# Optimization experiments

Measured on AMD Instinct MI355X. Metric: run time of the kernel, lower is better.

Reference implementation:

```python
import jax, jax.numpy as jnp
import numpy as np

N0, N1 = 30000, 20000
N = N0 + N1
E = 400000
H0, H1, H2 = 4, 4, 1
DH = 64            # num_hidden
NC = 16            # num_classes
IN = 128           # per-type input feature dim
SLOPE = 0.2        # leaky relu negative slope


def setup_inputs() -> dict:
    key = jax.random.key(0)
    ks = iter(jax.random.split(key, 48))
    rn = lambda shape, s=0.05: jax.random.normal(next(ks), shape, jnp.float32) * s
    ri = lambda shape: jax.random.randint(next(ks), shape, 0, N, jnp.int32)
    inp = {
        'features0': rn((N0, IN), 1.0),
        'features1': rn((N1, IN), 1.0),
        'fc_w0': rn((IN, DH)), 'fc_b0': jnp.zeros((DH,), jnp.float32),
        'fc_w1': rn((IN, DH)), 'fc_b1': jnp.zeros((DH,), jnp.float32),
        'mix_w': jnp.zeros((2, 3, 2), jnp.float32),  # (n_types, num_layers+1, n_graphs)
        # GATConv params stacked over the 2 relation graphs
        'W0': rn((2, DH, H0 * DH)), 'al0': rn((2, H0, DH), 0.1), 'ar0': rn((2, H0, DH), 0.1), 'b0': jnp.zeros((2, H0 * DH), jnp.float32),
        'W1': rn((2, H0 * DH, H1 * DH)), 'al1': rn((2, H1, DH), 0.1), 'ar1': rn((2, H1, DH), 0.1), 'b1': jnp.zeros((2, H1 * DH), jnp.float32),
        'W2': rn((2, H1 * DH, H2 * NC)), 'al2': rn((2, H2, NC), 0.1), 'ar2': rn((2, H2, NC), 0.1), 'b2': jnp.zeros((2, H2 * NC), jnp.float32),
        'res2': rn((2, H1 * DH, H2 * NC)),  # res_fc for last layer (in != out*heads)
        'src0': ri((E,)), 'dst0': ri((E,)),
        'src1': ri((E,)), 'dst1': ri((E,)),
    }
    return inp


def gat_conv(h, src, dst, W, al, ar, b, H, D, res_mode, res_w, act):
    # h: (N, in)  ->  (N, H, D)
    feat = (h @ W).reshape(N, H, D)
    el = jnp.sum(feat * al, axis=-1)   # (N, H)
    er = jnp.sum(feat * ar, axis=-1)   # (N, H)
    e = jax.nn.leaky_relu(el[src] + er[dst], SLOPE)  # (E, H)
    # edge softmax over incoming edges of each dst node
    m = jax.ops.segment_max(e, dst, num_segments=N)
    ex = jnp.exp(e - m[dst])
    den = jax.ops.segment_sum(ex, dst, num_segments=N)
    alpha = ex / den[dst]                              # (E, H)
    out = jax.ops.segment_sum(feat[src] * alpha[..., None], dst, num_segments=N)
    if res_mode == 'id':
        out = out + h.reshape(N, H, D)
    elif res_mode == 'fc':
        out = out + (h @ res_w).reshape(N, H, D)
    out = out + b.reshape(1, H, D)
    return jax.nn.elu(out) if act else out


def _forward(features0, features1, fc_w0, fc_b0, fc_w1, fc_b1, mix_w,
             W0, al0, ar0, b0, W1, al1, ar1, b1, W2, al2, ar2, b2, res2,
             src0, dst0, src1, dst1):
    nt = jnp.concatenate([jnp.zeros(N0, jnp.int32), jnp.ones(N1, jnp.int32)])
    w = jax.nn.softmax(mix_w, axis=2)  # (types, layers+1, graphs)
    h = jnp.concatenate([features0 @ fc_w0 + fc_b0, features1 @ fc_w1 + fc_b1], axis=0)
    srcs, dsts = (src0, src1), (dst0, dst1)
    layers = [
        (W0, al0, ar0, b0, H0, DH, None, True),
        (W1, al1, ar1, b1, H1, DH, 'id', True),
    ]
    for l, (W, al, ar, b, H, D, rm, act) in enumerate(layers):
        acc = 0.
        for i in range(2):
            o = gat_conv(h, srcs[i], dsts[i], W[i], al[i], ar[i], b[i], H, D, rm, None, act)
            acc = acc + o.reshape(N, H * D) * w[nt, l, i][:, None]
        h = acc
    logits = 0.
    for i in range(2):
        o = gat_conv(h, srcs[i], dsts[i], W2[i], al2[i], ar2[i], b2[i], H2, NC, 'fc', res2[i], False)
        logits = logits + o.mean(axis=1) * w[nt, 2, i][:, None]
    return logits


def reference(features0, features1, fc_w0, fc_b0, fc_w1, fc_b1, mix_w,
              W0, al0, ar0, b0, W1, al1, ar1, b1, W2, al2, ar2, b2, res2,
              src0, dst0, src1, dst1):
    return _forward(features0, features1, fc_w0, fc_b0, fc_w1, fc_b1, mix_w,
                    W0, al0, ar0, b0, W1, al1, ar1, b1, W2, al2, ar2, b2, res2,
                    src0, dst0, src1, dst1)
```

## Files before the change

kernel.cpp:

```cpp
#include <hip/hip_runtime.h>
#include <hip/hip_bf16.h>

#define NN   50000
#define NN0  30000
#define EE   400000
#define NB_SCAN ((NN + 1023) / 1024)
#define NRT   3125
#define NGRP  ((NRT + 3) / 4)

typedef unsigned short u16;
typedef unsigned int   u32;

typedef __attribute__((ext_vector_type(8))) __bf16 bf16x8;
typedef __attribute__((ext_vector_type(4))) float  f32x4;

__device__ __forceinline__ float bf2f(u16 u){ return __uint_as_float(((u32)u)<<16); }
__device__ __forceinline__ float lo16(u32 u){ return __uint_as_float(u<<16); }
__device__ __forceinline__ float hi16(u32 u){ return __uint_as_float(u & 0xffff0000u); }
__device__ __forceinline__ u16 f2bf(float f){
  u32 x = __float_as_uint(f);
  x += 0x7fffu + ((x>>16)&1u);
  return (u16)(x>>16);
}
__device__ __forceinline__ float elu_f(float x){ return x>0.f ? x : __expf(x)-1.f; }
__device__ __forceinline__ float lrelu(float x){ return x>0.f ? x : 0.2f*x; }
__device__ __forceinline__ bf16x8 ld_frag(const u16* p){
  uint4 v = *(const uint4*)p;
  return __builtin_bit_cast(bf16x8, v);
}

__global__ __launch_bounds__(256) void k_prep(
    const float* __restrict__ mix_w, float* __restrict__ wsoft,
    const float* __restrict__ W0, u16* __restrict__ W0p,
    const float* __restrict__ W1, u16* __restrict__ W1p,
    const float* __restrict__ W2, const float* __restrict__ res2, u16* __restrict__ W2p)
{
  int t = blockIdx.x*256 + threadIdx.x;
  if (t < 6){
    float a0 = mix_w[t*2+0], a1 = mix_w[t*2+1];
    float mx = fmaxf(a0,a1);
    float e0 = __expf(a0-mx), e1 = __expf(a1-mx);
    wsoft[t*2+0] = e0/(e0+e1); wsoft[t*2+1] = e1/(e0+e1);
  }
  if (t < 4096){
    int gg = t>>11, fi = t&2047;
    int lane = fi&63, kb = (fi>>6)&1, ct = fi>>7;
    int q = lane>>4, c = lane&15;
    const float* src = W0 + (size_t)gg*64*256;
    u16* o = W0p + (size_t)gg*16384 + (size_t)fi*8;
    #pragma unroll
    for (int j=0;j<8;j++) o[j] = f2bf(src[(size_t)(kb*32+q*8+j)*256 + ct*16 + c]);
  } else if (t < 20480){
    int u = t - 4096;
    int gg = u>>13, fi = u&8191;
    int lane = fi&63, kb = (fi>>6)&7, ct = fi>>9;
    int q = lane>>4, c = lane&15;
    const float* src = W1 + (size_t)gg*65536;
    u16* o = W1p + (size_t)gg*65536 + (size_t)fi*8;
    #pragma unroll
    for (int j=0;j<8;j++) o[j] = f2bf(src[(size_t)(kb*32+q*8+j)*256 + ct*16 + c]);
  } else if (t < 22528){
    int fi = t - 20480;
    int lane = fi&63, kb = (fi>>6)&7, ct = fi>>9;
    int q = lane>>4, c = lane&15;
    int cl = ct*16 + c;
    int i = cl>>5, which = (cl>>4)&1;
    const float* src = which ? res2 : W2;
    u16* o = W2p + (size_t)fi*8;
    #pragma unroll
    for (int j=0;j<8;j++) o[j] = f2bf(src[(size_t)i*4096 + (size_t)(kb*32+q*8+j)*16 + (cl&15)]);
  }
}

__global__ void k_count2(const int* __restrict__ d0, const int* __restrict__ d1,
                         int* __restrict__ cnt2){
  int t = blockIdx.x*256 + threadIdx.x;
  int g = blockIdx.y;
  if (t < EE) atomicAdd(&cnt2[g*NN + (g ? d1[t] : d0[t])], 1);
}

__global__ __launch_bounds__(1024) void k_scan1(const int* __restrict__ cnt2,
                                                int* __restrict__ row2, int* __restrict__ bsum){
  __shared__ int wsum[16];
  int g = blockIdx.y;
  int lane = threadIdx.x & 63, wid = threadIdx.x >> 6;
  int i = blockIdx.x*1024 + threadIdx.x;
  int v = (i < NN) ? cnt2[g*NN + i] : 0;
  int x = v;
  #pragma unroll
  for (int off = 1; off < 64; off <<= 1){
    int y = __shfl_up(x, off, 64);
    if (lane >= off) x += y;
  }
  if (lane == 63) wsum[wid] = x;
  __syncthreads();
  if (wid == 0 && lane < 16){
    int s = wsum[lane];
    #pragma unroll
    for (int off = 1; off < 16; off <<= 1){
      int y = __shfl_up(s, off, 16);
      if (lane >= off) s += y;
    }
    wsum[lane] = s;
  }
  __syncthreads();
  int incl = x + (wid ? wsum[wid-1] : 0);
  if (i < NN) row2[(size_t)g*(NN+1) + i] = incl - v;
  if (threadIdx.x == 1023) bsum[g*NB_SCAN + blockIdx.x] = incl;
}

__global__ __launch_bounds__(128) void k_scan2(const int* __restrict__ bsum, int* __restrict__ boff){
  int g = threadIdx.x >> 6, lane = threadIdx.x & 63;
  int v = (lane < NB_SCAN) ? bsum[g*NB_SCAN + lane] : 0;
  int x = v;
  #pragma unroll
  for (int off = 1; off < 64; off <<= 1){
    int y = __shfl_up(x, off, 64);
    if (lane >= off) x += y;
  }
  if (lane < NB_SCAN) boff[g*NB_SCAN + lane] = x - v;
}

__global__ __launch_bounds__(1024) void k_scan3(int* __restrict__ row2, const int* __restrict__ boff){
  int g = blockIdx.y;
  int i = blockIdx.x*1024 + threadIdx.x;
  if (i < NN) row2[(size_t)g*(NN+1) + i] += boff[g*NB_SCAN + blockIdx.x];
  if (blockIdx.x == 0 && threadIdx.x == 0) row2[(size_t)g*(NN+1) + NN] = EE;
}

__global__ void k_scatter2(const int* __restrict__ s0, const int* __restrict__ d0,
                           const int* __restrict__ s1, const int* __restrict__ d1,
                           const int* __restrict__ row2, int* __restrict__ fill2,
                           int* __restrict__ col2){
  int t = blockIdx.x*256 + threadIdx.x;
  int g = blockIdx.y;
  if (t >= EE) return;
  int d = g ? d1[t] : d0[t];
  int s = g ? s1[t] : s0[t];
  int pos = atomicAdd(&fill2[g*NN + d], 1);
  col2[(size_t)g*EE + row2[(size_t)g*(NN+1) + d] + pos] = s;
}

__global__ __launch_bounds__(256) void k_in_proj(
    const float* __restrict__ f0, const float* __restrict__ f1,
    const float* __restrict__ w0, const float* __restrict__ b0,
    const float* __restrict__ w1, const float* __restrict__ b1,
    u16* __restrict__ h)
{
  __shared__ float fs[4][128];
  int wv = threadIdx.x>>6, ln = threadIdx.x&63;
  int n = blockIdx.x*4 + wv;
  const float *fr, *W, *B;
  if (n < NN0){ fr = f0 + (size_t)n*128; W=w0; B=b0; }
  else        { fr = f1 + (size_t)(n-NN0)*128; W=w1; B=b1; }
  float2 u = ((const float2*)fr)[ln];
  fs[wv][2*ln]   = u.x;
  fs[wv][2*ln+1] = u.y;
  __syncthreads();
  float acc = B[ln];
  #pragma unroll 8
  for (int k=0;k<128;k++) acc = fmaf(fs[wv][k], W[k*64+ln], acc);
  h[(size_t)n*64 + ln] = f2bf(acc);
}

template<int K>
__global__ __launch_bounds__(256) void k_gemm4(
    const u16* __restrict__ A,
    const u16* __restrict__ Bp, size_t bpStride,
    const float* __restrict__ al, const float* __restrict__ ar, int alStride,
    u16* __restrict__ feat, size_t featStride,
    float* __restrict__ el, float* __restrict__ er, size_t elStride)
{
  constexpr int KB = K/32;
  int wv = threadIdx.x>>6, ln = threadIdx.x&63;
  int bid = blockIdx.x;
  int g = bid / NGRP, grp = bid % NGRP;
  int split = wv, q = ln>>4, c = ln&15;
  const u16* Bpg = Bp + (size_t)g*bpStride;
  const float* alg = al + (size_t)g*alStride;
  const float* arg = ar + (size_t)g*alStride;
  u16* featg = feat + (size_t)g*featStride;
  float* elg = el + (size_t)g*elStride;
  float* erg = er + (size_t)g*elStride;

  f32x4 acc[4][4] = {};
  int  tbase = grp*4;
  bool valid[4];
  const u16* Ap[4];
  #pragma unroll
  for (int rt=0; rt<4; rt++){
    int ti = tbase + rt;
    valid[rt] = (ti < NRT);
    if (!valid[rt]) ti = NRT-1;
    Ap[rt] = A + (size_t)(ti*16 + c)*K + q*8;
  }
  const u16* Bbase = Bpg + ((size_t)(split*4)*KB*64 + ln)*8;

  #pragma unroll 2
  for (int kb=0; kb<KB; kb++){
    bf16x8 b[4], a[4];
    #pragma unroll
    for (int ct=0; ct<4; ct++) b[ct] = ld_frag(Bbase + (size_t)(ct*KB + kb)*64*8);
    #pragma unroll
    for (int rt=0; rt<4; rt++) a[rt] = ld_frag(Ap[rt] + kb*32);
    #pragma unroll
    for (int rt=0; rt<4; rt++)
      #pragma unroll
      for (int ct=0; ct<4; ct++)
        acc[rt][ct] = __builtin_amdgcn_mfma_f32_16x16x32_bf16(a[rt], b[ct], acc[rt][ct], 0,0,0);
  }

  float alv[4], arv[4];
  #pragma unroll
  for (int ct=0;ct<4;ct++){
    int cg = (split*4+ct)*16 + c;
    alv[ct] = alg[cg]; arv[ct] = arg[cg];
  }
  #pragma unroll
  for (int rt=0; rt<4; rt++){
    if (!valid[rt]) continue;
    int row0 = (tbase+rt)*16;
    #pragma unroll
    for (int j=0;j<4;j++){
      float ep=0.f, rp=0.f;
      #pragma unroll
      for (int ct=0;ct<4;ct++){ ep += acc[rt][ct][j]*alv[ct]; rp += acc[rt][ct][j]*arv[ct]; }
      #pragma unroll
      for (int off=8; off; off>>=1){ ep += __shfl_xor(ep,off,16); rp += __shfl_xor(rp,off,16); }
      int row = row0 + q*4 + j;
      if (c==0){ elg[row*4+split]=ep; erg[row*4+split]=rp; }
      #pragma unroll
      for (int ct=0;ct<4;ct++)
        featg[(size_t)row*256 + (split*4+ct)*16 + c] = f2bf(acc[rt][ct][j]);
    }
  }
}

template<int RES>
__global__ __launch_bounds__(256) void k_aggNF(
    const int* __restrict__ row2, const int* __restrict__ col2,
    const u16* __restrict__ feat, size_t featStride,
    const float* __restrict__ el, const float* __restrict__ er, size_t elStride,
    const u16* __restrict__ hres, const float* __restrict__ bias,
    const float* __restrict__ wsoft, int l,
    u16* __restrict__ hout)
{
  int wv = threadIdx.x>>6, ln = threadIdx.x&63;
  int n = blockIdx.x*4 + wv;
  int h = ln>>4;
  int type = (n<NN0)?0:1;
  float rx=0.f, ry=0.f, rz=0.f, rw_=0.f;
  if (RES){
    uint2 r = ((const uint2*)hres)[(size_t)n*64 + ln];
    rx=lo16(r.x); ry=hi16(r.x); rz=lo16(r.y); rw_=hi16(r.y);
  }
  float o0=0.f,o1=0.f,o2=0.f,o3=0.f;
  #pragma unroll
  for (int g=0; g<2; g++){
    const int* rw = row2 + (size_t)g*(NN+1);
    const int* cl = col2 + (size_t)g*EE;
    const uint2* fp = (const uint2*)(feat + (size_t)g*featStride);
    const float* elg = el + (size_t)g*elStride;
    float er_h = (er + (size_t)g*elStride)[n*4+h];
    int beg = rw[n], end = rw[n+1];
    float den = 0.f;
    float a0=0.f,a1=0.f,a2=0.f,a3=0.f;
    int k = beg;
    for (; k+4<=end; k+=4){
      int s0=cl[k], s1=cl[k+1], s2=cl[k+2], s3=cl[k+3];
      float x0 = __expf(lrelu(elg[s0*4+h] + er_h));
      float x1 = __expf(lrelu(elg[s1*4+h] + er_h));
      float x2 = __expf(lrelu(elg[s2*4+h] + er_h));
      float x3 = __expf(lrelu(elg[s3*4+h] + er_h));
      uint2 f0 = fp[(size_t)s0*64 + ln];
      uint2 f1 = fp[(size_t)s1*64 + ln];
      uint2 f2 = fp[(size_t)s2*64 + ln];
      uint2 f3 = fp[(size_t)s3*64 + ln];
      den += (x0+x1) + (x2+x3);
      a0 += x0*lo16(f0.x) + x1*lo16(f1.x) + x2*lo16(f2.x) + x3*lo16(f3.x);
      a1 += x0*hi16(f0.x) + x1*hi16(f1.x) + x2*hi16(f2.x) + x3*hi16(f3.x);
      a2 += x0*lo16(f0.y) + x1*lo16(f1.y) + x2*lo16(f2.y) + x3*lo16(f3.y);
      a3 += x0*hi16(f0.y) + x1*hi16(f1.y) + x2*hi16(f2.y) + x3*hi16(f3.y);
    }
    for (; k<end; k++){
      int s = cl[k];
      float x = __expf(lrelu(elg[s*4+h] + er_h));
      uint2 f = fp[(size_t)s*64 + ln];
      den += x;
      a0 += x*lo16(f.x); a1 += x*hi16(f.x); a2 += x*lo16(f.y); a3 += x*hi16(f.y);
    }
    float inv = (end>beg) ? 1.0f/den : 0.f;
    float4 bv = ((const float4*)(bias + g*256))[ln];
    a0 = a0*inv + bv.x; a1 = a1*inv + bv.y; a2 = a2*inv + bv.z; a3 = a3*inv + bv.w;
    if (RES){ a0 += rx; a1 += ry; a2 += rz; a3 += rw_; }
    float w = wsoft[type*6 + l*2 + g];
    o0 += w*elu_f(a0); o1 += w*elu_f(a1); o2 += w*elu_f(a2); o3 += w*elu_f(a3);
  }
  uint2 o;
  o.x = (u32)f2bf(o0) | ((u32)f2bf(o1)<<16);
  o.y = (u32)f2bf(o2) | ((u32)f2bf(o3)<<16);
  ((uint2*)hout)[(size_t)n*64 + ln] = o;
}

template<int RES>
__global__ __launch_bounds__(256) void k_aggN(
    const int* __restrict__ row, const int* __restrict__ col,
    const u16* __restrict__ feat, const float* __restrict__ el, const float* __restrict__ er,
    const u16* __restrict__ hres, const float* __restrict__ bias,
    const float* __restrict__ wsoft, int l, int i, int first,
    u16* __restrict__ hout)
{
  int wv = threadIdx.x>>6, ln = threadIdx.x&63;
  int n = blockIdx.x*4 + wv;
  int h = ln>>4;
  int beg = row[n], end = row[n+1];
  float er_h = er[n*4+h];
  const uint2* fp = (const uint2*)feat;
  float den = 0.f;
  float a0=0.f,a1=0.f,a2=0.f,a3=0.f;
  int k = beg;
  for (; k+4<=end; k+=4){
    int s0=col[k], s1=col[k+1], s2=col[k+2], s3=col[k+3];
    float x0 = __expf(lrelu(el[s0*4+h] + er_h));
    float x1 = __expf(lrelu(el[s1*4+h] + er_h));
    float x2 = __expf(lrelu(el[s2*4+h] + er_h));
    float x3 = __expf(lrelu(el[s3*4+h] + er_h));
    uint2 f0 = fp[(size_t)s0*64 + ln];
    uint2 f1 = fp[(size_t)s1*64 + ln];
    uint2 f2 = fp[(size_t)s2*64 + ln];
    uint2 f3 = fp[(size_t)s3*64 + ln];
    den += (x0+x1) + (x2+x3);
    a0 += x0*lo16(f0.x) + x1*lo16(f1.x) + x2*lo16(f2.x) + x3*lo16(f3.x);
    a1 += x0*hi16(f0.x) + x1*hi16(f1.x) + x2*hi16(f2.x) + x3*hi16(f3.x);
    a2 += x0*lo16(f0.y) + x1*lo16(f1.y) + x2*lo16(f2.y) + x3*lo16(f3.y);
    a3 += x0*hi16(f0.y) + x1*hi16(f1.y) + x2*hi16(f2.y) + x3*hi16(f3.y);
  }
  for (; k<end; k++){
    int s = col[k];
    float x = __expf(lrelu(el[s*4+h] + er_h));
    uint2 f = fp[(size_t)s*64 + ln];
    den += x;
    a0 += x*lo16(f.x); a1 += x*hi16(f.x); a2 += x*lo16(f.y); a3 += x*hi16(f.y);
  }
  float inv = (end>beg) ? 1.0f/den : 0.f;
  a0 *= inv; a1 *= inv; a2 *= inv; a3 *= inv;
  float4 bv = ((const float4*)bias)[ln];
  a0 += bv.x; a1 += bv.y; a2 += bv.z; a3 += bv.w;
  if (RES){
    uint2 r = ((const uint2*)hres)[(size_t)n*64 + ln];
    a0 += lo16(r.x); a1 += hi16(r.x); a2 += lo16(r.y); a3 += hi16(r.y);
  }
  a0 = elu_f(a0); a1 = elu_f(a1); a2 = elu_f(a2); a3 = elu_f(a3);
  float w = wsoft[((n<NN0)?0:1)*6 + l*2 + i];
  a0 *= w; a1 *= w; a2 *= w; a3 *= w;
  if (!first){
    uint2 p = ((const uint2*)hout)[(size_t)n*64 + ln];
    a0 += lo16(p.x); a1 += hi16(p.x); a2 += lo16(p.y); a3 += hi16(p.y);
  }
  uint2 o;
  o.x = (u32)f2bf(a0) | ((u32)f2bf(a1)<<16);
  o.y = (u32)f2bf(a2) | ((u32)f2bf(a3)<<16);
  ((uint2*)hout)[(size_t)n*64 + ln] = o;
}

__global__ __launch_bounds__(256) void k_gemm2(
    const u16* __restrict__ A, const u16* __restrict__ Bp,
    const float* __restrict__ al2, const float* __restrict__ ar2,
    float* __restrict__ feat16, float* __restrict__ resb,
    float* __restrict__ el2, float* __restrict__ er2)
{
  int wv = threadIdx.x>>6, ln = threadIdx.x&63;
  int wt = blockIdx.x*4 + wv;
  if (wt >= NN/16) return;
  int row0 = wt*16;
  int q = ln>>4, c = ln&15;
  f32x4 acc[4] = {};
  const u16* Ap = A + (size_t)(row0 + c)*256 + q*8;
  #pragma unroll
  for (int kb=0; kb<8; kb++){
    bf16x8 a = ld_frag(Ap + kb*32);
    #pragma unroll
    for (int t=0;t<4;t++){
      bf16x8 b = ld_frag(Bp + ((size_t)(t*8 + kb)*64 + ln)*8);
      acc[t] = __builtin_amdgcn_mfma_f32_16x16x32_bf16(a, b, acc[t], 0,0,0);
    }
  }
  #pragma unroll
  for (int i=0;i<2;i++){
    float alv = al2[i*16+c], arv = ar2[i*16+c];
    #pragma unroll
    for (int j=0;j<4;j++){
      float ep = acc[2*i][j]*alv, rp = acc[2*i][j]*arv;
      #pragma unroll
      for (int off=8; off; off>>=1){ ep += __shfl_xor(ep,off,16); rp += __shfl_xor(rp,off,16); }
      if (c==0){
        int row = row0 + q*4 + j;
        el2[(size_t)i*NN + row] = ep; er2[(size_t)i*NN + row] = rp;
      }
    }
    #pragma unroll
    for (int j=0;j<4;j++){
      int row = row0 + q*4 + j;
      feat16[(size_t)i*NN*16 + (size_t)row*16 + c] = acc[2*i][j];
      resb  [(size_t)i*NN*16 + (size_t)row*16 + c] = acc[2*i+1][j];
    }
  }
}

__global__ __launch_bounds__(256) void k_agg2D(
    const int* __restrict__ row2, const int* __restrict__ col2,
    const float* __restrict__ feat16, const float* __restrict__ el2,
    const float* __restrict__ er2, const float* __restrict__ resb,
    const float* __restrict__ b2, const float* __restrict__ wsoft,
    float* __restrict__ out)
{
  int t = threadIdx.x;
  int nl = t>>4, j = t&15;
  int n = blockIdx.x*16 + nl;
  int type = (n<NN0)?0:1;
  float o = 0.f;
  #pragma unroll
  for (int i=0;i<2;i++){
    const int* rw = row2 + (size_t)i*(NN+1);
    const int* cl = col2 + (size_t)i*EE;
    const float* f  = feat16 + (size_t)i*NN*16;
    const float* eli= el2 + (size_t)i*NN;
    float ern = er2[(size_t)i*NN + n];
    int beg = rw[n], end = rw[n+1];
    float den = 0.f, acc = 0.f;
    int k = beg;
    for (; k+4<=end; k+=4){
      int s0=cl[k], s1=cl[k+1], s2=cl[k+2], s3=cl[k+3];
      float x0 = __expf(lrelu(eli[s0] + ern));
      float x1 = __expf(lrelu(eli[s1] + ern));
      float x2 = __expf(lrelu(eli[s2] + ern));
      float x3 = __expf(lrelu(eli[s3] + ern));
      float v0 = f[(size_t)s0*16 + j];
      float v1 = f[(size_t)s1*16 + j];
      float v2 = f[(size_t)s2*16 + j];
      float v3 = f[(size_t)s3*16 + j];
      den += (x0+x1) + (x2+x3);
      acc += x0*v0 + x1*v1 + x2*v2 + x3*v3;
    }
    for (; k<end; k++){
      int s = cl[k];
      float x = __expf(lrelu(eli[s] + ern));
      den += x;
      acc = fmaf(x, f[(size_t)s*16 + j], acc);
    }
    float inv = (end>beg) ? 1.0f/den : 0.f;
    float oi = acc*inv + b2[i*16+j] + resb[(size_t)i*NN*16 + (size_t)n*16 + j];
    o += oi * wsoft[type*6 + 4 + i];
  }
  out[(size_t)n*16 + j] = o;
}

extern "C" void kernel_launch(void* const* d_in, const int* in_sizes, int n_in,
                              void* d_out, int out_size, void* d_ws, size_t ws_size,
                              hipStream_t stream)
{
  const float* features0 = (const float*)d_in[0];
  const float* features1 = (const float*)d_in[1];
  const float* fc_w0 = (const float*)d_in[2];
  const float* fc_b0 = (const float*)d_in[3];
  const float* fc_w1 = (const float*)d_in[4];
  const float* fc_b1 = (const float*)d_in[5];
  const float* mix_w = (const float*)d_in[6];
  const float* W0  = (const float*)d_in[7];
  const float* al0 = (const float*)d_in[8];
  const float* ar0 = (const float*)d_in[9];
  const float* b0  = (const float*)d_in[10];
  const float* W1  = (const float*)d_in[11];
  const float* al1 = (const float*)d_in[12];
  const float* ar1 = (const float*)d_in[13];
  const float* b1  = (const float*)d_in[14];
  const float* W2  = (const float*)d_in[15];
  const float* al2 = (const float*)d_in[16];
  const float* ar2 = (const float*)d_in[17];
  const float* b2  = (const float*)d_in[18];
  const float* res2= (const float*)d_in[19];
  const int* src[2] = {(const int*)d_in[20], (const int*)d_in[22]};
  const int* dst[2] = {(const int*)d_in[21], (const int*)d_in[23]};
  (void)in_sizes; (void)n_in; (void)out_size;

  char* ws = (char*)d_ws;
  size_t off = 0;
  auto alloc = [&](size_t bytes)->char*{
    char* p = ws + off; off += (bytes + 255) & ~(size_t)255; return p;
  };
  float* wsoft = (float*)alloc(64*4);
  u16*   W0p   = (u16*)  alloc((size_t)2*64*256*2);
  u16*   W1p   = (u16*)  alloc((size_t)2*256*256*2);
  u16*   W2p   = (u16*)  alloc((size_t)256*64*2);
  int*   row2  = (int*)  alloc((size_t)2*(NN+1)*4);
  int*   col2  = (int*)  alloc((size_t)2*EE*4);
  int*   zeros = (int*)  alloc((size_t)4*NN*4);
  int*   cnt2  = zeros;
  int*   fill2 = zeros + 2*NN;
  int*   bsum  = (int*)alloc((size_t)2*NB_SCAN*4);
  int*   boff  = (int*)alloc((size_t)2*NB_SCAN*4);
  u16*   h0    = (u16*)alloc((size_t)NN*64*2);
  u16*   h1    = (u16*)alloc((size_t)NN*256*2);
  u16*   h2    = (u16*)alloc((size_t)NN*256*2);
  float* elA   = (float*)alloc((size_t)2*NN*4*4);
  float* erA   = (float*)alloc((size_t)2*NN*4*4);
  size_t featBytes1 = (size_t)NN*256*2;
  size_t off_D = off;
  bool fused = (ws_size >= off_D + 2*featBytes1 + (16<<20));
  u16* featD = (u16*)alloc(fused ? 2*featBytes1 : featBytes1);
  float* feat16 = (float*)(ws + off_D);
  float* resb   = feat16 + (size_t)2*NN*16;
  float* el2    = resb   + (size_t)2*NN*16;
  float* er2    = el2    + (size_t)2*NN;

  k_prep<<<(22528+255)/256,256,0,stream>>>(mix_w, wsoft, W0, W0p, W1, W1p, W2, res2, W2p);

  hipMemsetAsync(zeros, 0, (size_t)4*NN*4, stream);
  {
    dim3 gE((EE+255)/256, 2), gS(NB_SCAN, 2);
    k_count2 <<<gE,256,0,stream>>>(dst[0], dst[1], cnt2);
    k_scan1  <<<gS,1024,0,stream>>>(cnt2, row2, bsum);
    k_scan2  <<<1,128,0,stream>>>(bsum, boff);
    k_scan3  <<<gS,1024,0,stream>>>(row2, boff);
    k_scatter2<<<gE,256,0,stream>>>(src[0], dst[0], src[1], dst[1], row2, fill2, col2);
  }

  k_in_proj<<<NN/4,256,0,stream>>>(features0, features1, fc_w0, fc_b0, fc_w1, fc_b1, h0);

  if (fused){
    k_gemm4<64><<<2*NGRP,256,0,stream>>>(h0, W0p, (size_t)64*256, al0, ar0, 256,
                                         featD, featBytes1/2, elA, erA, (size_t)NN*4);
    k_aggNF<0><<<NN/4,256,0,stream>>>(row2, col2, featD, featBytes1/2, elA, erA, (size_t)NN*4,
                                      (const u16*)nullptr, b0, wsoft, 0, h1);
    k_gemm4<256><<<2*NGRP,256,0,stream>>>(h1, W1p, (size_t)256*256, al1, ar1, 256,
                                          featD, featBytes1/2, elA, erA, (size_t)NN*4);
    k_aggNF<1><<<NN/4,256,0,stream>>>(row2, col2, featD, featBytes1/2, elA, erA, (size_t)NN*4,
                                      h1, b1, wsoft, 1, h2);
  } else {
    for (int i=0;i<2;i++){
      k_gemm4<64><<<NGRP,256,0,stream>>>(h0, W0p+(size_t)i*64*256, 0, al0+i*256, ar0+i*256, 0,
                                         featD, 0, elA, erA, 0);
      k_aggN<0><<<NN/4,256,0,stream>>>(row2+(size_t)i*(NN+1), col2+(size_t)i*EE, featD, elA, erA,
                                       (const u16*)nullptr, b0+i*256, wsoft, 0, i, (i==0)?1:0, h1);
    }
    for (int i=0;i<2;i++){
      k_gemm4<256><<<NGRP,256,0,stream>>>(h1, W1p+(size_t)i*256*256, 0, al1+i*256, ar1+i*256, 0,
                                          featD, 0, elA, erA, 0);
      k_aggN<1><<<NN/4,256,0,stream>>>(row2+(size_t)i*(NN+1), col2+(size_t)i*EE, featD, elA, erA,
                                       h1, b1+i*256, wsoft, 1, i, (i==0)?1:0, h2);
    }
  }

  k_gemm2<<<(NN/16+3)/4,256,0,stream>>>(h2, W2p, al2, ar2, feat16, resb, el2, er2);
  k_agg2D<<<NN/16,256,0,stream>>>(row2, col2, feat16, el2, er2, resb, b2, wsoft, (float*)d_out);
}
```

Before: 496.8 us.

## Aggregate layer-0 in 64-dim input space before projecting with W0

Layer 0 now aggregates the 64-wide h0 features per head (edge softmax applied) and only then multiplies by W0, using linearity of the projection. The attention logits el/er come from h0 through precomputed folded vectors W0·al / W0·ar, so the 256-wide per-graph feature tensor is no longer gathered during aggregation. The input projection moves to MFMA bf16, which converts the features to bf16 on the fly. The change adds an intermediate aggB buffer, three kernels replacing two, and removes the non-fused fallback path, so the fused workspace size is now assumed.

Measured after the change: 465.9 us. 1.07x faster.

```diff
diff --git a/kernel.cpp b/kernel.cpp
--- a/kernel.cpp
+++ b/kernel.cpp
@@ -7,6 +7,7 @@
 #define NB_SCAN ((NN + 1023) / 1024)
 #define NRT   3125
 #define NGRP  ((NRT + 3) / 4)
+#define NT0   1875
 
 typedef unsigned short u16;
 typedef unsigned int   u32;
@@ -28,12 +29,24 @@
   uint4 v = *(const uint4*)p;
   return __builtin_bit_cast(bf16x8, v);
 }
+__device__ __forceinline__ bf16x8 cvt8(const float* p){
+  float4 u = ((const float4*)p)[0];
+  float4 v = ((const float4*)p)[1];
+  u32 w0 = (u32)f2bf(u.x) | ((u32)f2bf(u.y)<<16);
+  u32 w1 = (u32)f2bf(u.z) | ((u32)f2bf(u.w)<<16);
+  u32 w2 = (u32)f2bf(v.x) | ((u32)f2bf(v.y)<<16);
+  u32 w3 = (u32)f2bf(v.z) | ((u32)f2bf(v.w)<<16);
+  uint4 r{w0,w1,w2,w3};
+  return __builtin_bit_cast(bf16x8, r);
+}
 
 __global__ __launch_bounds__(256) void k_prep(
     const float* __restrict__ mix_w, float* __restrict__ wsoft,
     const float* __restrict__ W0, u16* __restrict__ W0p,
     const float* __restrict__ W1, u16* __restrict__ W1p,
-    const float* __restrict__ W2, const float* __restrict__ res2, u16* __restrict__ W2p)
+    const float* __restrict__ W2, const float* __restrict__ res2, u16* __restrict__ W2p,
+    const float* __restrict__ fcw0, const float* __restrict__ fcw1, u16* __restrict__ Fp,
+    const float* __restrict__ al0, const float* __restrict__ ar0, u16* __restrict__ Vp)
 {
   int t = blockIdx.x*256 + threadIdx.x;
   if (t < 6){
@@ -46,7 +59,7 @@
     int gg = t>>11, fi = t&2047;
     int lane = fi&63, kb = (fi>>6)&1, ct = fi>>7;
     int q = lane>>4, c = lane&15;
-    const float* src = W0 + (size_t)gg*64*256;
+    const float* src = W0 + (size_t)gg*16384;
     u16* o = W0p + (size_t)gg*16384 + (size_t)fi*8;
     #pragma unroll
     for (int j=0;j<8;j++) o[j] = f2bf(src[(size_t)(kb*32+q*8+j)*256 + ct*16 + c]);
@@ -69,6 +82,28 @@
     u16* o = W2p + (size_t)fi*8;
     #pragma unroll
     for (int j=0;j<8;j++) o[j] = f2bf(src[(size_t)i*4096 + (size_t)(kb*32+q*8+j)*16 + (cl&15)]);
+  } else if (t < 24576){
+    int u = t - 22528;
+    int tt = u>>10, fi = u&1023;
+    int lane = fi&63, kb = (fi>>6)&3, ct = fi>>8;
+    int q = lane>>4, c = lane&15;
+    const float* src = tt ? fcw1 : fcw0;
+    u16* o = Fp + (size_t)tt*8192 + (size_t)fi*8;
+    #pragma unroll
+    for (int j=0;j<8;j++) o[j] = f2bf(src[(size_t)(kb*32+q*8+j)*64 + ct*16 + c]);
+  } else if (t < 25600){
+    int u = t - 24576;
+    int fi = u>>3, j = u&7;
+    int lane = fi&63, kb = fi>>6;
+    int q = lane>>4, c = lane&15;
+    int k = kb*32 + q*8 + j;
+    int which = c>>3, g=(c>>2)&1, h=c&3;
+    const float* sel = (which ? ar0 : al0) + (size_t)(g*4+h)*64;
+    const float* Wrow = W0 + (size_t)g*16384 + (size_t)k*256 + h*64;
+    float s=0.f;
+    #pragma unroll 8
+    for (int d=0;d<64;d++) s = fmaf(Wrow[d], sel[d], s);
+    Vp[(size_t)fi*8 + j] = f2bf(s);
   }
 }
 
@@ -141,26 +176,158 @@
   col2[(size_t)g*EE + row2[(size_t)g*(NN+1) + d] + pos] = s;
 }
 
-__global__ __launch_bounds__(256) void k_in_proj(
+__global__ __launch_bounds__(256) void k_inproj_m(
     const float* __restrict__ f0, const float* __restrict__ f1,
-    const float* __restrict__ w0, const float* __restrict__ b0,
-    const float* __restrict__ w1, const float* __restrict__ b1,
-    u16* __restrict__ h)
-{
-  __shared__ float fs[4][128];
+    const u16* __restrict__ Fp, const float* __restrict__ fb0, const float* __restrict__ fb1,
+    u16* __restrict__ h0)
+{
+  int wv = threadIdx.x>>6, ln = threadIdx.x&63;
+  int ti = blockIdx.x*4 + wv;
+  if (ti >= NRT) return;
+  int q = ln>>4, c = ln&15;
+  int type = (ti < NT0) ? 0 : 1;
+  const float* F = type ? f1 : f0;
+  int rbase = type ? (ti*16 - NN0) : ti*16;
+  const u16* Bg = Fp + (size_t)type*8192;
+  const float* bb = type ? fb1 : fb0;
+  f32x4 acc[4] = {};
+  const float* Ap = F + (size_t)(rbase + c)*128;
+  #pragma unroll
+  for (int kb=0; kb<4; kb++){
+    bf16x8 a = cvt8(Ap + kb*32 + q*8);
+    #pragma unroll
+    for (int ct=0; ct<4; ct++){
+      bf16x8 b = ld_frag(Bg + ((size_t)(ct*4+kb)*64 + ln)*8);
+      acc[ct] = __builtin_amdgcn_mfma_f32_16x16x32_bf16(a, b, acc[ct], 0,0,0);
+    }
+  }
+  #pragma unroll
+  for (int ct=0; ct<4; ct++){
+    float bv = bb[ct*16+c];
+    #pragma unroll
+    for (int j=0;j<4;j++){
+      int row = ti*16 + q*4 + j;
+      h0[(size_t)row*64 + ct*16 + c] = f2bf(acc[ct][j] + bv);
+    }
+  }
+}
+
+__global__ __launch_bounds__(256) void k_eler0(
+    const u16* __restrict__ h0, const u16* __restrict__ Vp,
+    float* __restrict__ elA, float* __restrict__ erA)
+{
+  int wv = threadIdx.x>>6, ln = threadIdx.x&63;
+  int ti = blockIdx.x*4 + wv;
+  if (ti >= NRT) return;
+  int q = ln>>4, c = ln&15;
+  f32x4 acc = {};
+  const u16* Ap = h0 + (size_t)(ti*16 + c)*64 + q*8;
+  #pragma unroll
+  for (int kb=0; kb<2; kb++){
+    bf16x8 a = ld_frag(Ap + kb*32);
+    bf16x8 b = ld_frag(Vp + ((size_t)(kb*64 + ln))*8);
+    acc = __builtin_amdgcn_mfma_f32_16x16x32_bf16(a, b, acc, 0,0,0);
+  }
+  int which = c>>3, g = (c>>2)&1, h = c&3;
+  float* dst = (which ? erA : elA) + (size_t)g*NN*4;
+  #pragma unroll
+  for (int j=0;j<4;j++){
+    int row = ti*16 + q*4 + j;
+    dst[row*4 + h] = acc[j];
+  }
+}
+
+__global__ __launch_bounds__(256) void k_agg0(
+    const int* __restrict__ row2, const int* __restrict__ col2,
+    const u16* __restrict__ h0,
+    const float* __restrict__ elA, const float* __restrict__ erA,
+    u16* __restrict__ aggB, size_t aggStride)
+{
   int wv = threadIdx.x>>6, ln = threadIdx.x&63;
   int n = blockIdx.x*4 + wv;
-  const float *fr, *W, *B;
-  if (n < NN0){ fr = f0 + (size_t)n*128; W=w0; B=b0; }
-  else        { fr = f1 + (size_t)(n-NN0)*128; W=w1; B=b1; }
-  float2 u = ((const float2*)fr)[ln];
-  fs[wv][2*ln]   = u.x;
-  fs[wv][2*ln+1] = u.y;
-  __syncthreads();
-  float acc = B[ln];
-  #pragma unroll 8
-  for (int k=0;k<128;k++) acc = fmaf(fs[wv][k], W[k*64+ln], acc);
-  h[(size_t)n*64 + ln] = f2bf(acc);
+  #pragma unroll
+  for (int g=0; g<2; g++){
+    const int* rw = row2 + (size_t)g*(NN+1);
+    const int* cl = col2 + (size_t)g*EE;
+    const float* elg = elA + (size_t)g*NN*4;
+    float4 er4 = ((const float4*)(erA + (size_t)g*NN*4))[n];
+    int beg = rw[n], end = rw[n+1];
+    float d0=0.f,d1=0.f,d2=0.f,d3=0.f;
+    float a0=0.f,a1=0.f,a2=0.f,a3=0.f;
+    int k = beg;
+    for (; k+2<=end; k+=2){
+      int s0 = cl[k], s1 = cl[k+1];
+      float4 e0 = ((const float4*)elg)[s0];
+      float4 e1 = ((const float4*)elg)[s1];
+      float v0 = bf2f(h0[(size_t)s0*64 + ln]);
+      float v1 = bf2f(h0[(size_t)s1*64 + ln]);
+      float x00=__expf(lrelu(e0.x+er4.x)), x01=__expf(lrelu(e0.y+er4.y));
+      float x02=__expf(lrelu(e0.z+er4.z)), x03=__expf(lrelu(e0.w+er4.w));
+      float x10=__expf(lrelu(e1.x+er4.x)), x11=__expf(lrelu(e1.y+er4.y));
+      float x12=__expf(lrelu(e1.z+er4.z)), x13=__expf(lrelu(e1.w+er4.w));
+      d0 += x00+x10; d1 += x01+x11; d2 += x02+x12; d3 += x03+x13;
+      a0 += x00*v0 + x10*v1; a1 += x01*v0 + x11*v1;
+      a2 += x02*v0 + x12*v1; a3 += x03*v0 + x13*v1;
+    }
+    for (; k<end; k++){
+      int s = cl[k];
+      float4 e0 = ((const float4*)elg)[s];
+      float v = bf2f(h0[(size_t)s*64 + ln]);
+      float x0=__expf(lrelu(e0.x+er4.x)), x1=__expf(lrelu(e0.y+er4.y));
+      float x2=__expf(lrelu(e0.z+er4.z)), x3=__expf(lrelu(e0.w+er4.w));
+      d0+=x0; d1+=x1; d2+=x2; d3+=x3;
+      a0+=x0*v; a1+=x1*v; a2+=x2*v; a3+=x3*v;
+    }
+    bool has = (end > beg);
+    a0 = has ? a0/d0 : 0.f; a1 = has ? a1/d1 : 0.f;
+    a2 = has ? a2/d2 : 0.f; a3 = has ? a3/d3 : 0.f;
+    u16* og = aggB + (size_t)g*aggStride + (size_t)n*256 + ln;
+    og[0]   = f2bf(a0); og[64]  = f2bf(a1);
+    og[128] = f2bf(a2); og[192] = f2bf(a3);
+  }
+}
+
+__global__ __launch_bounds__(256) void k_head0(
+    const u16* __restrict__ aggB, size_t aggStride,
+    const u16* __restrict__ W0p, const float* __restrict__ b0,
+    const float* __restrict__ wsoft, u16* __restrict__ h1)
+{
+  int wv = threadIdx.x>>6, ln = threadIdx.x&63;
+  int ti = blockIdx.x*4 + wv;
+  if (ti >= NRT) return;
+  int q = ln>>4, c = ln&15;
+  int type = (ti < NT0) ? 0 : 1;
+  float wg0 = wsoft[type*6 + 0];
+  float wg1 = wsoft[type*6 + 1];
+  for (int h=0; h<4; h++){
+    f32x4 acc[2][4] = {};
+    #pragma unroll
+    for (int g=0; g<2; g++){
+      const u16* Ap = aggB + (size_t)g*aggStride + (size_t)(ti*16 + c)*256 + h*64 + q*8;
+      const u16* Bg = W0p + (size_t)g*16384;
+      #pragma unroll
+      for (int kb=0; kb<2; kb++){
+        bf16x8 a = ld_frag(Ap + kb*32);
+        #pragma unroll
+        for (int ct=0; ct<4; ct++){
+          int ctg = h*4 + ct;
+          bf16x8 b = ld_frag(Bg + ((size_t)(ctg*2 + kb)*64 + ln)*8);
+          acc[g][ct] = __builtin_amdgcn_mfma_f32_16x16x32_bf16(a, b, acc[g][ct], 0,0,0);
+        }
+      }
+    }
+    #pragma unroll
+    for (int ct=0; ct<4; ct++){
+      int colg = h*64 + ct*16 + c;
+      float bb0 = b0[colg], bb1 = b0[256 + colg];
+      #pragma unroll
+      for (int j=0;j<4;j++){
+        int row = ti*16 + q*4 + j;
+        float o = wg0*elu_f(acc[0][ct][j] + bb0) + wg1*elu_f(acc[1][ct][j] + bb1);
+        h1[(size_t)row*256 + colg] = f2bf(o);
+      }
+    }
+  }
 }
 
 template<int K>
@@ -302,67 +469,6 @@
   ((uint2*)hout)[(size_t)n*64 + ln] = o;
 }
 
-template<int RES>
-__global__ __launch_bounds__(256) void k_aggN(
-    const int* __restrict__ row, const int* __restrict__ col,
-    const u16* __restrict__ feat, const float* __restrict__ el, const float* __restrict__ er,
-    const u16* __restrict__ hres, const float* __restrict__ bias,
-    const float* __restrict__ wsoft, int l, int i, int first,
-    u16* __restrict__ hout)
-{
-  int wv = threadIdx.x>>6, ln = threadIdx.x&63;
-  int n = blockIdx.x*4 + wv;
-  int h = ln>>4;
-  int beg = row[n], end = row[n+1];
-  float er_h = er[n*4+h];
-  const uint2* fp = (const uint2*)feat;
-  float den = 0.f;
-  float a0=0.f,a1=0.f,a2=0.f,a3=0.f;
-  int k = beg;
-  for (; k+4<=end; k+=4){
-    int s0=col[k], s1=col[k+1], s2=col[k+2], s3=col[k+3];
-    float x0 = __expf(lrelu(el[s0*4+h] + er_h));
-    float x1 = __expf(lrelu(el[s1*4+h] + er_h));
-    float x2 = __expf(lrelu(el[s2*4+h] + er_h));
-    float x3 = __expf(lrelu(el[s3*4+h] + er_h));
-    uint2 f0 = fp[(size_t)s0*64 + ln];
-    uint2 f1 = fp[(size_t)s1*64 + ln];
-    uint2 f2 = fp[(size_t)s2*64 + ln];
-    uint2 f3 = fp[(size_t)s3*64 + ln];
-    den += (x0+x1) + (x2+x3);
-    a0 += x0*lo16(f0.x) + x1*lo16(f1.x) + x2*lo16(f2.x) + x3*lo16(f3.x);
-    a1 += x0*hi16(f0.x) + x1*hi16(f1.x) + x2*hi16(f2.x) + x3*hi16(f3.x);
-    a2 += x0*lo16(f0.y) + x1*lo16(f1.y) + x2*lo16(f2.y) + x3*lo16(f3.y);
-    a3 += x0*hi16(f0.y) + x1*hi16(f1.y) + x2*hi16(f2.y) + x3*hi16(f3.y);
-  }
-  for (; k<end; k++){
-    int s = col[k];
-    float x = __expf(lrelu(el[s*4+h] + er_h));
-    uint2 f = fp[(size_t)s*64 + ln];
-    den += x;
-    a0 += x*lo16(f.x); a1 += x*hi16(f.x); a2 += x*lo16(f.y); a3 += x*hi16(f.y);
-  }
-  float inv = (end>beg) ? 1.0f/den : 0.f;
-  a0 *= inv; a1 *= inv; a2 *= inv; a3 *= inv;
-  float4 bv = ((const float4*)bias)[ln];
-  a0 += bv.x; a1 += bv.y; a2 += bv.z; a3 += bv.w;
-  if (RES){
-    uint2 r = ((const uint2*)hres)[(size_t)n*64 + ln];
-    a0 += lo16(r.x); a1 += hi16(r.x); a2 += lo16(r.y); a3 += hi16(r.y);
-  }
-  a0 = elu_f(a0); a1 = elu_f(a1); a2 = elu_f(a2); a3 = elu_f(a3);
-  float w = wsoft[((n<NN0)?0:1)*6 + l*2 + i];
-  a0 *= w; a1 *= w; a2 *= w; a3 *= w;
-  if (!first){
-    uint2 p = ((const uint2*)hout)[(size_t)n*64 + ln];
-    a0 += lo16(p.x); a1 += hi16(p.x); a2 += lo16(p.y); a3 += hi16(p.y);
-  }
-  uint2 o;
-  o.x = (u32)f2bf(a0) | ((u32)f2bf(a1)<<16);
-  o.y = (u32)f2bf(a2) | ((u32)f2bf(a3)<<16);
-  ((uint2*)hout)[(size_t)n*64 + ln] = o;
-}
-
 __global__ __launch_bounds__(256) void k_gemm2(
     const u16* __restrict__ A, const u16* __restrict__ Bp,
     const float* __restrict__ al2, const float* __restrict__ ar2,
@@ -371,7 +477,7 @@
 {
   int wv = threadIdx.x>>6, ln = threadIdx.x&63;
   int wt = blockIdx.x*4 + wv;
-  if (wt >= NN/16) return;
+  if (wt >= NRT) return;
   int row0 = wt*16;
   int q = ln>>4, c = ln&15;
   f32x4 acc[4] = {};
@@ -481,7 +587,7 @@
   const float* res2= (const float*)d_in[19];
   const int* src[2] = {(const int*)d_in[20], (const int*)d_in[22]};
   const int* dst[2] = {(const int*)d_in[21], (const int*)d_in[23]};
-  (void)in_sizes; (void)n_in; (void)out_size;
+  (void)in_sizes; (void)n_in; (void)out_size; (void)ws_size;
 
   char* ws = (char*)d_ws;
   size_t off = 0;
@@ -492,6 +598,8 @@
   u16*   W0p   = (u16*)  alloc((size_t)2*64*256*2);
   u16*   W1p   = (u16*)  alloc((size_t)2*256*256*2);
   u16*   W2p   = (u16*)  alloc((size_t)256*64*2);
+  u16*   Fp    = (u16*)  alloc((size_t)2*128*64*2);
+  u16*   Vp    = (u16*)  alloc((size_t)64*16*2);
   int*   row2  = (int*)  alloc((size_t)2*(NN+1)*4);
   int*   col2  = (int*)  alloc((size_t)2*EE*4);
   int*   zeros = (int*)  alloc((size_t)4*NN*4);
@@ -504,16 +612,18 @@
   u16*   h2    = (u16*)alloc((size_t)NN*256*2);
   float* elA   = (float*)alloc((size_t)2*NN*4*4);
   float* erA   = (float*)alloc((size_t)2*NN*4*4);
-  size_t featBytes1 = (size_t)NN*256*2;
+  size_t featStride = (size_t)NN*256;
   size_t off_D = off;
-  bool fused = (ws_size >= off_D + 2*featBytes1 + (16<<20));
-  u16* featD = (u16*)alloc(fused ? 2*featBytes1 : featBytes1);
+  u16* regionD = (u16*)alloc(2*featStride*2);
+  u16* aggB  = regionD;
+  u16* featD = regionD;
   float* feat16 = (float*)(ws + off_D);
   float* resb   = feat16 + (size_t)2*NN*16;
   float* el2    = resb   + (size_t)2*NN*16;
   float* er2    = el2    + (size_t)2*NN;
 
-  k_prep<<<(22528+255)/256,256,0,stream>>>(mix_w, wsoft, W0, W0p, W1, W1p, W2, res2, W2p);
+  k_prep<<<100,256,0,stream>>>(mix_w, wsoft, W0, W0p, W1, W1p, W2, res2, W2p,
+                               fc_w0, fc_w1, Fp, al0, ar0, Vp);
 
   hipMemsetAsync(zeros, 0, (size_t)4*NN*4, stream);
   {
@@ -525,32 +635,17 @@
     k_scatter2<<<gE,256,0,stream>>>(src[0], dst[0], src[1], dst[1], row2, fill2, col2);
   }
 
-  k_in_proj<<<NN/4,256,0,stream>>>(features0, features1, fc_w0, fc_b0, fc_w1, fc_b1, h0);
-
-  if (fused){
-    k_gemm4<64><<<2*NGRP,256,0,stream>>>(h0, W0p, (size_t)64*256, al0, ar0, 256,
-                                         featD, featBytes1/2, elA, erA, (size_t)NN*4);
-    k_aggNF<0><<<NN/4,256,0,stream>>>(row2, col2, featD, featBytes1/2, elA, erA, (size_t)NN*4,
-                                      (const u16*)nullptr, b0, wsoft, 0, h1);
-    k_gemm4<256><<<2*NGRP,256,0,stream>>>(h1, W1p, (size_t)256*256, al1, ar1, 256,
-                                          featD, featBytes1/2, elA, erA, (size_t)NN*4);
-    k_aggNF<1><<<NN/4,256,0,stream>>>(row2, col2, featD, featBytes1/2, elA, erA, (size_t)NN*4,
-                                      h1, b1, wsoft, 1, h2);
-  } else {
-    for (int i=0;i<2;i++){
-      k_gemm4<64><<<NGRP,256,0,stream>>>(h0, W0p+(size_t)i*64*256, 0, al0+i*256, ar0+i*256, 0,
-                                         featD, 0, elA, erA, 0);
-      k_aggN<0><<<NN/4,256,0,stream>>>(row2+(size_t)i*(NN+1), col2+(size_t)i*EE, featD, elA, erA,
-                                       (const u16*)nullptr, b0+i*256, wsoft, 0, i, (i==0)?1:0, h1);
-    }
-    for (int i=0;i<2;i++){
-      k_gemm4<256><<<NGRP,256,0,stream>>>(h1, W1p+(size_t)i*256*256, 0, al1+i*256, ar1+i*256, 0,
-                                          featD, 0, elA, erA, 0);
-      k_aggN<1><<<NN/4,256,0,stream>>>(row2+(size_t)i*(NN+1), col2+(size_t)i*EE, featD, elA, erA,
-                                       h1, b1+i*256, wsoft, 1, i, (i==0)?1:0, h2);
-    }
-  }
-
-  k_gemm2<<<(NN/16+3)/4,256,0,stream>>>(h2, W2p, al2, ar2, feat16, resb, el2, er2);
+  k_inproj_m<<<NGRP,256,0,stream>>>(features0, features1, Fp, fc_b0, fc_b1, h0);
+  k_eler0   <<<NGRP,256,0,stream>>>(h0, Vp, elA, erA);
+
+  k_agg0 <<<NN/4,256,0,stream>>>(row2, col2, h0, elA, erA, aggB, featStride);
+  k_head0<<<NGRP,256,0,stream>>>(aggB, featStride, W0p, b0, wsoft, h1);
+
+  k_gemm4<256><<<2*NGRP,256,0,stream>>>(h1, W1p, (size_t)256*256, al1, ar1, 256,
+                                        featD, featStride, elA, erA, (size_t)NN*4);
+  k_aggNF<1><<<NN/4,256,0,stream>>>(row2, col2, featD, featStride, elA, erA, (size_t)NN*4,
+                                    h1, b1, wsoft, 1, h2);
+
+  k_gemm2<<<NGRP,256,0,stream>>>(h2, W2p, al2, ar2, feat16, resb, el2, er2);
   k_agg2D<<<NN/16,256,0,stream>>>(row2, col2, feat16, el2, er2, resb, b2, wsoft, (float*)d_out);
 }
```
